# Kernel tuning notes

Measured on AMD Instinct MI355X. Metric: run time of the kernel, lower is better.

The kernel has to match this reference:

```python
import jax, jax.numpy as jnp
from jax import lax
import numpy as np

EPS = 1e-6
LN_EPS = 1e-3
B, T, F = 8, 2048, 80
STRIDE, NFILT = 2, 64
FEAT_P = 20              # ceil(80 / 4) after two stride-2 convs
CAPS_IN_N, CAPS_IN_D = 32, 8
CAPS_COV_N, CAPS_COV_D = 32, 8
CLASS_N, CAPS_CLS_D = 31, 8
WINDOW, LPAD, RPAD = 3, 1, 1
N_ITER = 3


def conv2d(x, w, b, stride):
    y = lax.conv_general_dilated(x, w, (stride, stride), 'SAME',
                                 dimension_numbers=('NHWC', 'HWIO', 'NHWC'))
    return y + b


def feat_mask(x, lengths, factor):
    # zero out time steps >= ceil(len/factor)
    S = x.shape[1]
    vl = jnp.ceil(lengths.astype(jnp.float32) / factor).astype(jnp.int32)
    m = (jnp.arange(S)[None, :] < vl[:, None]).astype(x.dtype)
    return x * m.reshape(m.shape + (1,) * (x.ndim - 2))


def squash(x, axis=-1):
    sq = jnp.sum(x * x, axis=axis, keepdims=True)
    return x * (sq / (1.0 + sq) / jnp.sqrt(sq + EPS))


def layernorm(x):
    mu = jnp.mean(x, -1, keepdims=True)
    var = jnp.var(x, -1, keepdims=True)
    return (x - mu) / jnp.sqrt(var + LN_EPS)


def window_concat(x):
    # [B,S,N,D] -> [B,S,N*WINDOW,D] (windowed context gather)
    S = x.shape[1]
    xp = jnp.pad(x, ((0, 0), (LPAD, RPAD), (0, 0), (0, 0)))
    return jnp.concatenate([xp[:, j:j + S] for j in range(WINDOW)], axis=2)


def dynamic_routing(u_hat, logit_mask):
    # u_hat: [B,S,I,O,D] -> v: [B,S,O,D]
    b0 = jnp.zeros(u_hat.shape[:4], u_hat.dtype)

    def body(b, _):
        c = jax.nn.softmax(b + logit_mask, axis=3)          # coupling coeffs
        s = jnp.einsum('bsio,bsiod->bsod', c, u_hat)
        v = squash(s, -1)
        b = b + jnp.einsum('bsiod,bsod->bsio', u_hat, v)    # agreement update
        return b, v

    _, vs = lax.scan(body, b0, None, length=N_ITER)
    return vs[-1]


def _forward(inputs, conv0_w1, conv0_b1, conv0_w2, conv0_b2,
             conv1_w1, conv1_b1, conv1_w2, conv1_b2,
             proj_w, proj_b, enc_w1, enc_b1, enc_w2, enc_b2,
             W0, B0, W1, B1, input_lengths):
    # --- CapsulationLayer: maxout conv feature extraction ---
    x = inputs[..., None]                                    # [B,T,F,1]
    x = jnp.maximum(conv2d(x, conv0_w1, conv0_b1, STRIDE),
                    conv2d(x, conv0_w2, conv0_b2, STRIDE))
    x = feat_mask(x, input_lengths, STRIDE)                  # [B,T/2,F/2,64]
    x = jnp.maximum(conv2d(x, conv1_w1, conv1_b1, STRIDE),
                    conv2d(x, conv1_w2, conv1_b2, STRIDE))
    x = feat_mask(x, input_lengths, STRIDE ** 2)             # [B,S,20,64]
    b, S = x.shape[0], x.shape[1]

    # --- primary capsules ---
    emb = x.reshape(b, S, FEAT_P * NFILT) @ proj_w + proj_b  # [B,S,32]
    emb = emb[..., None]                                     # [B,S,32,1]
    emb = jnp.maximum(conv2d(emb, enc_w1, enc_b1, 1),
                      conv2d(emb, enc_w2, enc_b2, 1))        # [B,S,32,8]
    emb = feat_mask(emb, input_lengths, STRIDE ** 2)
    emb = squash(emb, -1)
    emb = layernorm(emb.reshape(b, S, -1)).reshape(b, S, CAPS_IN_N, CAPS_IN_D)

    # --- caps layer 0: primary(windowed) -> convolution capsules ---
    win = window_concat(emb)                                 # [B,S,96,8]
    u = jnp.einsum('iodk,bsik->bsiod', W0, win) + B0[None, None]
    v = dynamic_routing(u, jnp.zeros((1, 1, 1, CAPS_COV_N), u.dtype))
    emb = layernorm(v.reshape(b, S, -1)).reshape(b, S, CAPS_COV_N, CAPS_COV_D)

    # --- caps layer 1: conv(windowed) -> class capsules (blank masked) ---
    win = window_concat(emb)                                 # [B,S,96,8]
    u = jnp.einsum('iodk,bsik->bsiod', W1, win) + B1[None, None]
    lm = jnp.concatenate([jnp.full((1, 1, 1, 1), -1e9, u.dtype),
                          jnp.zeros((1, 1, 1, CLASS_N - 1), u.dtype)], -1)
    v = dynamic_routing(u, lm)
    v = layernorm(v.reshape(b, S, -1)).reshape(b, S, CLASS_N, CAPS_CLS_D)

    # --- class capsule lengths + output layernorm ---
    out = jnp.sqrt(jnp.sum(v * v, -1) + EPS)                 # [B,S,31]
    return layernorm(out)


def setup_inputs() -> dict:
    key = jax.random.key(0)
    ks = list(jax.random.split(key, 24))
    n = lambda i, shape, s=0.1: jax.random.normal(ks[i], shape, jnp.float32) * s
    d = {
        'inputs': jax.random.normal(ks[0], (B, T, F), jnp.float32),
        'conv0_w1': n(1, (3, 3, 1, NFILT)), 'conv0_b1': n(2, (NFILT,)),
        'conv0_w2': n(3, (3, 3, 1, NFILT)), 'conv0_b2': n(4, (NFILT,)),
        'conv1_w1': n(5, (3, 3, NFILT, NFILT), 0.05), 'conv1_b1': n(6, (NFILT,)),
        'conv1_w2': n(7, (3, 3, NFILT, NFILT), 0.05), 'conv1_b2': n(8, (NFILT,)),
        'proj_w': n(9, (FEAT_P * NFILT, CAPS_IN_N), 0.02), 'proj_b': n(10, (CAPS_IN_N,)),
        'enc_w1': n(11, (3, 3, 1, CAPS_IN_D)), 'enc_b1': n(12, (CAPS_IN_D,)),
        'enc_w2': n(13, (3, 3, 1, CAPS_IN_D)), 'enc_b2': n(14, (CAPS_IN_D,)),
        'W0': n(15, (CAPS_IN_N * WINDOW, CAPS_COV_N, CAPS_COV_D, CAPS_IN_D)),
        'B0': n(16, (CAPS_IN_N * WINDOW, CAPS_COV_N, CAPS_COV_D)),
        'W1': n(17, (CAPS_COV_N * WINDOW, CLASS_N, CAPS_CLS_D, CAPS_COV_D)),
        'B1': n(18, (CAPS_COV_N * WINDOW, CLASS_N, CAPS_CLS_D)),
        'input_lengths': jax.random.randint(ks[19], (B,), T // 2, T + 1, jnp.int32),
    }
    return d


def reference(inputs, conv0_w1, conv0_b1, conv0_w2, conv0_b2,
              conv1_w1, conv1_b1, conv1_w2, conv1_b2,
              proj_w, proj_b, enc_w1, enc_b1, enc_w2, enc_b2,
              W0, B0, W1, B1, input_lengths):
    return _forward(inputs, conv0_w1, conv0_b1, conv0_w2, conv0_b2,
                    conv1_w1, conv1_b1, conv1_w2, conv1_b2,
                    proj_w, proj_b, enc_w1, enc_b1, enc_w2, enc_b2,
                    W0, B0, W1, B1, input_lengths)
```

## Files before the change

kernel.cpp:

```cpp
#include <hip/hip_runtime.h>

typedef unsigned short u16;
typedef unsigned int u32;
typedef short short8 __attribute__((ext_vector_type(8)));
typedef float f32x4 __attribute__((ext_vector_type(4)));
typedef _Float16 h2 __attribute__((ext_vector_type(2)));
typedef __fp16 fp16v2 __attribute__((ext_vector_type(2)));

#define DEV static __device__ __forceinline__

DEV float bf2f(u16 v) { return __uint_as_float((u32)v << 16); }
DEV u16 f2bf(float f) {
    u32 x = __float_as_uint(f);
    return (u16)((x + 0x7fffu + ((x >> 16) & 1u)) >> 16);
}
DEV u16 f2h(float f) {
    union { _Float16 h; u16 u; } c; c.h = (_Float16)f; return c.u;
}
DEV u32 pack2h(float a, float b) {
#if __has_builtin(__builtin_amdgcn_cvt_pkrtz)
    union { fp16v2 h; u32 u; } c;
    c.h = __builtin_amdgcn_cvt_pkrtz(a, b);
    return c.u;
#else
    union { u32 u; _Float16 h[2]; } c;
    c.h[0] = (_Float16)a; c.h[1] = (_Float16)b; return c.u;
#endif
}
DEV h2 u2h(u32 x) { union { u32 u; h2 h; } c; c.u = x; return c.h; }
DEV u32 h2u(h2 v) { union { h2 h; u32 u; } c; c.h = v; return c.u; }

#if __has_builtin(__builtin_amdgcn_fdot2)
DEV float dot2(u32 a, u32 b, float c) {
    return __builtin_amdgcn_fdot2(u2h(a), u2h(b), c, false);
}
#else
DEV float dot2(u32 a, u32 b, float c) {
    h2 ha = u2h(a), hb = u2h(b);
    c = fmaf((float)ha[0], (float)hb[0], c);
    return fmaf((float)ha[1], (float)hb[1], c);
}
#endif

constexpr int Bn = 8, Tn = 2048, Fn = 80, NF = 64;
constexpr int H1 = 1024, W1n = 40;
constexpr int Sn = 512,  W2n = 20;
constexpr int PK = 1280;
constexpr int I0 = 96;
constexpr int O0 = 32;
constexpr int O1 = 31;
constexpr int CPW = 52;
constexpr int NW0 = I0 * O0 * 8 * 8;
constexpr int NW1 = I0 * O1 * 8 * 8;
constexpr int KC1 = 576;

template <int CTRL>
DEV float dpp_mov(float x) {
    return __int_as_float(__builtin_amdgcn_update_dpp(
        0, __float_as_int(x), CTRL, 0xF, 0xF, true));
}
template <int CTRL>
DEV u32 dppu(u32 x) {
    return (u32)__builtin_amdgcn_update_dpp(0, (int)x, CTRL, 0xF, 0xF, true);
}
DEV float sum8(float x) {
    x += dpp_mov<0xB1>(x);
    x += dpp_mov<0x4E>(x);
    x += dpp_mov<0x141>(x);
    return x;
}
DEV u32 sum8h(u32 x) {
    x = h2u(u2h(x) + u2h(dppu<0xB1>(x)));
    x = h2u(u2h(x) + u2h(dppu<0x4E>(x)));
    x = h2u(u2h(x) + u2h(dppu<0x141>(x)));
    return x;
}

DEV float2 block_sum2(float a, float b, int tid, float* lds ) {
    #pragma unroll
    for (int m = 1; m < 64; m <<= 1) {
        a += __shfl_xor(a, m);
        b += __shfl_xor(b, m);
    }
    int wid = tid >> 6;
    __syncthreads();
    if ((tid & 63) == 0) { lds[wid * 2] = a; lds[wid * 2 + 1] = b; }
    __syncthreads();
    float ra = lds[0] + lds[2] + lds[4] + lds[6];
    float rb = lds[1] + lds[3] + lds[5] + lds[7];
    return make_float2(ra, rb);
}

__global__ void __launch_bounds__(256) k_prep(
        const float* __restrict__ w0, const float* __restrict__ w1c,
        const float* __restrict__ cw1, const float* __restrict__ cb1,
        const float* __restrict__ cw2, const float* __restrict__ cb2,
        u16* __restrict__ w0h, u16* __restrict__ w1h,
        u16* __restrict__ wt, float* __restrict__ biasi) {
    int idx = blockIdx.x * 256 + threadIdx.x;
    if (idx < NW0) w0h[idx] = f2h(w0[idx]);
    if (idx < NW1) w1h[idx] = f2h(w1c[idx]);
    if (idx < 128 * KC1) {
        int n = idx / KC1, k = idx - n * KC1;
        int c = n >> 1, s = n & 1;
        const float* w = s ? cw2 : cw1;
        wt[idx] = f2bf(w[k * 64 + c]);
    }
    if (idx < 128) {
        int c = idx >> 1, s = idx & 1;
        biasi[idx] = (s ? cb2 : cb1)[c];
    }
}

__global__ void __launch_bounds__(256) k_conv0(
        const float* __restrict__ in,
        const float* __restrict__ w1, const float* __restrict__ b1,
        const float* __restrict__ w2, const float* __restrict__ b2,
        const int* __restrict__ lens, u16* __restrict__ x1) {
    int idx = blockIdx.x * 256 + threadIdx.x;
    if (idx >= Bn * H1 * W1n * NF) return;
    int c = idx & 63;
    int rest = idx >> 6;
    int w = rest % W1n; rest /= W1n;
    int h = rest % H1;
    int b = rest / H1;
    float out = 0.f;
    int vl2 = (lens[b] + 1) >> 1;
    if (h < vl2) {
        float a1 = b1[c], a2 = b2[c];
        #pragma unroll
        for (int r = 0; r < 3; ++r) {
            int t = 2 * h + r;
            if (t < Tn) {
                #pragma unroll
                for (int q = 0; q < 3; ++q) {
                    int f = 2 * w + q;
                    if (f < Fn) {
                        float v = in[(b * Tn + t) * Fn + f];
                        int wi = (r * 3 + q) * 64 + c;
                        a1 = fmaf(v, w1[wi], a1);
                        a2 = fmaf(v, w2[wi], a2);
                    }
                }
            }
        }
        out = fmaxf(a1, a2);
    }
    x1[idx] = f2bf(out);
}

__global__ void __launch_bounds__(256) k_conv1(
        const u16* __restrict__ x1, const u16* __restrict__ wt,
        const float* __restrict__ biasi, const int* __restrict__ lens,
        u16* __restrict__ x2) {
    constexpr int LD = 40;
    __shared__ u16 Al[2][128 * LD];
    __shared__ u16 Bl[2][128 * LD];
    __shared__ float bs_lds[128];

    int tid = threadIdx.x;
    int m0 = blockIdx.x * 128;
    int b = m0 / 10240;
    int vl4 = (lens[b] + 3) >> 2;

    if (tid < 128) bs_lds[tid] = biasi[tid];

    int srow = tid >> 1;
    int shalf = tid & 1;
    int am = m0 + srow;
    int aw = am % 20;
    int ah = (am / 20) % 512;
    const u16* abase = x1 + (((size_t)b * 1024 + 2 * ah) * 40 + 2 * aw) * 64;
    const u16* bbase = wt + srow * KC1;

    const uint4 uz = make_uint4(0, 0, 0, 0);
    uint4 na0, na1, nb0, nb1;
    {
        const u16* ap = abase + shalf * 16;
        na0 = *(const uint4*)(ap);
        na1 = *(const uint4*)(ap + 8);
        const u16* bp = bbase + shalf * 16;
        nb0 = *(const uint4*)(bp);
        nb1 = *(const uint4*)(bp + 8);
    }
    {
        u16* awp = &Al[0][srow * LD + shalf * 16];
        *(uint4*)awp = na0; *(uint4*)(awp + 8) = na1;
        u16* bwp = &Bl[0][srow * LD + shalf * 16];
        *(uint4*)bwp = nb0; *(uint4*)(bwp + 8) = nb1;
    }
    __syncthreads();

    int lane = tid & 63;
    int wid = tid >> 6;
    int mw = wid & 1, nw = wid >> 1;
    int frow = lane & 15;
    int koff = (lane >> 4) * 8;

    f32x4 acc[4][4] = {};
    int buf = 0;

    #pragma unroll
    for (int kc = 0; kc < 18; ++kc) {
        if (kc < 17) {
            int kn = kc + 1;
            int rq = kn >> 1, ci0 = (kn & 1) * 32;
            int r = rq / 3, q = rq - 3 * r;
            bool v = (2 * ah + r < 1024) && (2 * aw + q < 40);
            const u16* ap = abase + (r * 40 + q) * 64 + ci0 + shalf * 16;
            na0 = v ? *(const uint4*)(ap) : uz;
            na1 = v ? *(const uint4*)(ap + 8) : uz;
            const u16* bp = bbase + kn * 32 + shalf * 16;
            nb0 = *(const uint4*)(bp);
            nb1 = *(const uint4*)(bp + 8);
        }
        const u16* Ar = &Al[buf][(mw * 64 + frow) * LD + koff];
        const u16* Br = &Bl[buf][(nw * 64 + frow) * LD + koff];
        short8 af[4], bfr[4];
        #pragma unroll
        for (int s = 0; s < 4; ++s) {
            af[s]  = *(const short8*)(Ar + s * 16 * LD);
            bfr[s] = *(const short8*)(Br + s * 16 * LD);
        }
        #pragma unroll
        for (int sm = 0; sm < 4; ++sm)
            #pragma unroll
            for (int sn = 0; sn < 4; ++sn)
                acc[sm][sn] = __builtin_amdgcn_mfma_f32_16x16x32_bf16(
                    af[sm], bfr[sn], acc[sm][sn], 0, 0, 0);
        if (kc < 17) {
            buf ^= 1;
            u16* awp = &Al[buf][srow * LD + shalf * 16];
            *(uint4*)awp = na0; *(uint4*)(awp + 8) = na1;
            u16* bwp = &Bl[buf][srow * LD + shalf * 16];
            *(uint4*)bwp = nb0; *(uint4*)(bwp + 8) = nb1;
            __syncthreads();
        }
    }

    int orow = (lane >> 4) * 4;
    int ncol = lane & 15;
    #pragma unroll
    for (int sm = 0; sm < 4; ++sm) {
        #pragma unroll
        for (int sn = 0; sn < 4; ++sn) {
            int np = nw * 64 + sn * 16 + ncol;
            float bia = bs_lds[np];
            #pragma unroll
            for (int r = 0; r < 4; ++r) {
                float v = acc[sm][sn][r] + bia;
                float o = fmaxf(v, dpp_mov<0xB1>(v));
                if (!(lane & 1)) {
                    int gm = m0 + mw * 64 + sm * 16 + orow + r;
                    int w = gm % 20;
                    int h = (gm / 20) % 512;
                    float res = (h >= vl4) ? 0.f : o;
                    x2[((size_t)(b * 512 + h) * 20 + w) * 64 + (np >> 1)] = f2bf(res);
                }
            }
        }
    }
}

__global__ void __launch_bounds__(256) k_proj(
        const u16* __restrict__ x2, const float* __restrict__ pw,
        const float* __restrict__ pb, float* __restrict__ proj) {
    int bs = blockIdx.x;
    int tid = threadIdx.x;
    int o = tid & 31, part = tid >> 5;
    const u16* row = &x2[(size_t)bs * PK];
    float acc = 0.f;
    int k0 = part * 160;
    #pragma unroll 8
    for (int k = 0; k < 160; ++k)
        acc = fmaf(bf2f(row[k0 + k]), pw[(k0 + k) * 32 + o], acc);
    __shared__ float red[256];
    red[tid] = acc;
    __syncthreads();
    if (tid < 32) {
        float s = 0.f;
        #pragma unroll
        for (int p = 0; p < 8; ++p) s += red[p * 32 + tid];
        proj[bs * 32 + tid] = s + pb[tid];
    }
}

__global__ void __launch_bounds__(256) k_enc(
        const float* __restrict__ proj,
        const float* __restrict__ ew1, const float* __restrict__ eb1,
        const float* __restrict__ ew2, const float* __restrict__ eb2,
        const int* __restrict__ lens, float* __restrict__ emb0) {
    int bs = blockIdx.x;
    int s = bs & (Sn - 1);
    int b = bs >> 9;
    int tid = threadIdx.x;
    __shared__ float rows[3][32];
    __shared__ float red[8];
    if (tid < 96) {
        int r = tid >> 5, n = tid & 31;
        int sr = s - 1 + r;
        rows[r][n] = (sr >= 0 && sr < Sn) ? proj[(b * Sn + sr) * 32 + n] : 0.f;
    }
    __syncthreads();

    int n = tid >> 3, d = tid & 7;
    float a1 = eb1[d], a2 = eb2[d];
    #pragma unroll
    for (int r = 0; r < 3; ++r) {
        #pragma unroll
        for (int q = 0; q < 3; ++q) {
            int nn = n - 1 + q;
            if (nn >= 0 && nn < 32) {
                float v = rows[r][nn];
                int wi = (r * 3 + q) * 8 + d;
                a1 = fmaf(v, ew1[wi], a1);
                a2 = fmaf(v, ew2[wi], a2);
            }
        }
    }
    float x = fmaxf(a1, a2);
    int vl4 = (lens[b] + 3) >> 2;
    if (s >= vl4) x = 0.f;

    float sq = sum8(x * x);
    x = x * (sq / (1.f + sq) * rsqrtf(sq + 1e-6f));

    float2 ss = block_sum2(x, x * x, tid, red);
    float mu = ss.x * (1.f / 256.f);
    float var = ss.y * (1.f / 256.f) - mu * mu;
    emb0[bs * 256 + tid] = (x - mu) * rsqrtf(var + 1e-3f);
}

__global__ void __launch_bounds__(256, 3) k_caps0(
        const float* __restrict__ embin, const u16* __restrict__ W0,
        const float* __restrict__ B0, float* __restrict__ embout) {
    int pb2 = blockIdx.x;
    int b = pb2 >> 8;
    int s0 = (pb2 & 255) << 1;
    int tid = threadIdx.x;
    int o = tid >> 3;

    __shared__ __align__(16) u32 win2[2][I0 * 4];
    __shared__ float blog[2][I0 * 33];
    __shared__ __align__(16) u32 cpk[2][O0 * CPW];
    __shared__ float red[8];
    u16* cph0 = (u16*)cpk[0];
    u16* cph1 = (u16*)cpk[1];

    for (int idx = tid; idx < 2 * I0 * 4; idx += 256) {
        int g = idx >= I0 * 4;
        int lidx = idx - g * I0 * 4;
        int i = lidx >> 2, kk = lidx & 3;
        int sr = s0 + g + (i >> 5) - 1;
        float a = 0.f, bv = 0.f;
        if (sr >= 0 && sr < Sn) {
            const float* p = &embin[(b * Sn + sr) * 256 + (i & 31) * 8 + kk * 2];
            a = p[0]; bv = p[1];
        }
        win2[g][lidx] = pack2h(a, bv);
    }
    for (int i = tid; i < 2 * I0 * 33; i += 256) blog[0][i] = 0.f;
    __syncthreads();

    u32 u_pk0[48], u_pk1[48];
    {
        const uint4* Wv = (const uint4*)W0;
        const uint4* wl0 = (const uint4*)win2[0];
        const uint4* wl1 = (const uint4*)win2[1];
        #pragma unroll
        for (int ii = 0; ii < 48; ++ii) {
            int i0 = 2 * ii, i1 = 2 * ii + 1;
            uint4 wv0 = Wv[i0 * 256 + tid];
            uint4 wv1 = Wv[i1 * 256 + tid];
            float bb0 = B0[i0 * 256 + tid];
            float bb1 = B0[i1 * 256 + tid];
            uint4 wa0 = wl0[i0], wa1 = wl0[i1];
            float a0 = bb0, a1 = bb1;
            a0 = dot2(wv0.x, wa0.x, a0);
            a0 = dot2(wv0.y, wa0.y, a0);
            a0 = dot2(wv0.z, wa0.z, a0);
            a0 = dot2(wv0.w, wa0.w, a0);
            a1 = dot2(wv1.x, wa1.x, a1);
            a1 = dot2(wv1.y, wa1.y, a1);
            a1 = dot2(wv1.z, wa1.z, a1);
            a1 = dot2(wv1.w, wa1.w, a1);
            u_pk0[ii] = pack2h(a0, a1);
            uint4 wb0 = wl1[i0], wb1 = wl1[i1];
            a0 = bb0; a1 = bb1;
            a0 = dot2(wv0.x, wb0.x, a0);
            a0 = dot2(wv0.y, wb0.y, a0);
            a0 = dot2(wv0.z, wb0.z, a0);
            a0 = dot2(wv0.w, wb0.w, a0);
            a1 = dot2(wv1.x, wb1.x, a1);
            a1 = dot2(wv1.y, wb1.y, a1);
            a1 = dot2(wv1.z, wb1.z, a1);
            a1 = dot2(wv1.w, wb1.w, a1);
            u_pk1[ii] = pack2h(a0, a1);
        }
    }

    float vv0 = 0.f, vv1 = 0.f;
    for (int it = 0; it < 3; ++it) {
        if (tid < 192) {
            int i = tid >> 1, hf = tid & 1;
            int o0 = hf * 16;
            #pragma unroll
            for (int g = 0; g < 2; ++g) {
                float ex[16];
                float ssum = 0.f;
                #pragma unroll
                for (int j = 0; j < 16; ++j) {
                    ex[j] = __expf(blog[g][i * 33 + o0 + j]);
                    ssum += ex[j];
                }
                ssum += dpp_mov<0xB1>(ssum);
                float inv = __builtin_amdgcn_rcpf(ssum);
                u16* cc = g ? cph1 : cph0;
                #pragma unroll
                for (int j = 0; j < 16; ++j)
                    cc[(o0 + j) * (CPW * 2) + i] = f2h(ex[j] * inv);
            }
        }
        __syncthreads();
        {
            float sv0 = 0.f, sv1 = 0.f;
            const uint4* cr0 = (const uint4*)&cpk[0][o * CPW];
            const uint4* cr1 = (const uint4*)&cpk[1][o * CPW];
            #pragma unroll
            for (int q4 = 0; q4 < 12; ++q4) {
                uint4 c0 = cr0[q4], c1 = cr1[q4];
                sv0 = dot2(u_pk0[q4 * 4 + 0], c0.x, sv0);
                sv0 = dot2(u_pk0[q4 * 4 + 1], c0.y, sv0);
                sv0 = dot2(u_pk0[q4 * 4 + 2], c0.z, sv0);
                sv0 = dot2(u_pk0[q4 * 4 + 3], c0.w, sv0);
                sv1 = dot2(u_pk1[q4 * 4 + 0], c1.x, sv1);
                sv1 = dot2(u_pk1[q4 * 4 + 1], c1.y, sv1);
                sv1 = dot2(u_pk1[q4 * 4 + 2], c1.z, sv1);
                sv1 = dot2(u_pk1[q4 * 4 + 3], c1.w, sv1);
            }
            float sq0 = sum8(sv0 * sv0);
            float sq1 = sum8(sv1 * sv1);
            vv0 = sv0 * (sq0 / (1.f + sq0) * rsqrtf(sq0 + 1e-6f));
            vv1 = sv1 * (sq1 / (1.f + sq1) * rsqrtf(sq1 + 1e-6f));
        }
        if (it < 2) {
            u32 va = pack2h(vv0, vv0), vb = pack2h(vv1, vv1);
            #pragma unroll
            for (int ii = 0; ii < 48; ++ii) {
                u32 p0 = sum8h(h2u(u2h(u_pk0[ii]) * u2h(va)));
                u32 p1 = sum8h(h2u(u2h(u_pk1[ii]) * u2h(vb)));
                if ((tid & 7) == 0) {
                    h2 q0 = u2h(p0), q1 = u2h(p1);
                    blog[0][(2 * ii) * 33 + o]     += (float)q0[0];
                    blog[0][(2 * ii + 1) * 33 + o] += (float)q0[1];
                    blog[1][(2 * ii) * 33 + o]     += (float)q1[0];
                    blog[1][(2 * ii + 1) * 33 + o] += (float)q1[1];
                }
            }
            __syncthreads();
        }
    }

    float2 ss = block_sum2(vv0, vv0 * vv0, tid, red);
    float mu = ss.x * (1.f / 256.f);
    float var = ss.y * (1.f / 256.f) - mu * mu;
    embout[(b * Sn + s0) * 256 + tid] = (vv0 - mu) * rsqrtf(var + 1e-3f);
    ss = block_sum2(vv1, vv1 * vv1, tid, red);
    mu = ss.x * (1.f / 256.f);
    var = ss.y * (1.f / 256.f) - mu * mu;
    embout[(b * Sn + s0 + 1) * 256 + tid] = (vv1 - mu) * rsqrtf(var + 1e-3f);
}

__global__ void __launch_bounds__(256, 3) k_caps1(
        const float* __restrict__ embin, const u16* __restrict__ W1,
        const float* __restrict__ B1, float* __restrict__ outp) {
    int pb2 = blockIdx.x;
    int b = pb2 >> 8;
    int s0 = (pb2 & 255) << 1;
    int tid = threadIdx.x;
    int o = tid >> 3, d = tid & 7;
    bool valid = (o < O1);
    int oc = valid ? o : (O1 - 1);
    int ocd = oc * 8 + d;

    __shared__ __align__(16) u32 win2[2][I0 * 4];
    __shared__ float blog[2][I0 * 33];
    __shared__ __align__(16) u32 cpk[2][O1 * CPW];
    __shared__ float red[8];
    __shared__ float lenb[2][O1];
    __shared__ float mv2[4];
    u16* cph0 = (u16*)cpk[0];
    u16* cph1 = (u16*)cpk[1];

    for (int idx = tid; idx < 2 * I0 * 4; idx += 256) {
        int g = idx >= I0 * 4;
        int lidx = idx - g * I0 * 4;
        int i = lidx >> 2, kk = lidx & 3;
        int sr = s0 + g + (i >> 5) - 1;
        float a = 0.f, bv = 0.f;
        if (sr >= 0 && sr < Sn) {
            const float* p = &embin[(b * Sn + sr) * 256 + (i & 31) * 8 + kk * 2];
            a = p[0]; bv = p[1];
        }
        win2[g][lidx] = pack2h(a, bv);
    }
    for (int i = tid; i < 2 * I0 * 33; i += 256) blog[0][i] = 0.f;
    for (int i = tid; i < CPW; i += 256) { cpk[0][i] = 0; cpk[1][i] = 0; }
    __syncthreads();

    u32 u_pk0[48], u_pk1[48];
    {
        const uint4* Wv = (const uint4*)W1;
        const uint4* wl0 = (const uint4*)win2[0];
        const uint4* wl1 = (const uint4*)win2[1];
        #pragma unroll
        for (int ii = 0; ii < 48; ++ii) {
            int i0 = 2 * ii, i1 = 2 * ii + 1;
            uint4 wv0 = Wv[i0 * 248 + ocd];
            uint4 wv1 = Wv[i1 * 248 + ocd];
            float bb0 = B1[i0 * 248 + ocd];
            float bb1 = B1[i1 * 248 + ocd];
            uint4 wa0 = wl0[i0], wa1 = wl0[i1];
            float a0 = bb0, a1 = bb1;
            a0 = dot2(wv0.x, wa0.x, a0);
            a0 = dot2(wv0.y, wa0.y, a0);
            a0 = dot2(wv0.z, wa0.z, a0);
            a0 = dot2(wv0.w, wa0.w, a0);
            a1 = dot2(wv1.x, wa1.x, a1);
            a1 = dot2(wv1.y, wa1.y, a1);
            a1 = dot2(wv1.z, wa1.z, a1);
            a1 = dot2(wv1.w, wa1.w, a1);
            u_pk0[ii] = pack2h(a0, a1);
            uint4 wb0 = wl1[i0], wb1 = wl1[i1];
            a0 = bb0; a1 = bb1;
            a0 = dot2(wv0.x, wb0.x, a0);
            a0 = dot2(wv0.y, wb0.y, a0);
            a0 = dot2(wv0.z, wb0.z, a0);
            a0 = dot2(wv0.w, wb0.w, a0);
            a1 = dot2(wv1.x, wb1.x, a1);
            a1 = dot2(wv1.y, wb1.y, a1);
            a1 = dot2(wv1.z, wb1.z, a1);
            a1 = dot2(wv1.w, wb1.w, a1);
            u_pk1[ii] = pack2h(a0, a1);
        }
    }

    float vv0 = 0.f, vv1 = 0.f;
    for (int it = 0; it < 3; ++it) {
        if (tid < 192) {
            int i = tid >> 1, hf = tid & 1;
            int lo = hf ? 16 : 1;
            #pragma unroll
            for (int g = 0; g < 2; ++g) {
                float ex[15];
                float ssum = 0.f;
                #pragma unroll
                for (int j = 0; j < 15; ++j) {
                    ex[j] = __expf(blog[g][i * 33 + lo + j]);
                    ssum += ex[j];
                }
                ssum += dpp_mov<0xB1>(ssum);
                float inv = __builtin_amdgcn_rcpf(ssum);
                u16* cc = g ? cph1 : cph0;
                #pragma unroll
                for (int j = 0; j < 15; ++j)
                    cc[(lo + j) * (CPW * 2) + i] = f2h(ex[j] * inv);
            }
        }
        __syncthreads();
        {
            float sv0 = 0.f, sv1 = 0.f;
            const uint4* cr0 = (const uint4*)&cpk[0][oc * CPW];
            const uint4* cr1 = (const uint4*)&cpk[1][oc * CPW];
            #pragma unroll
            for (int q4 = 0; q4 < 12; ++q4) {
                uint4 c0 = cr0[q4], c1 = cr1[q4];
                sv0 = dot2(u_pk0[q4 * 4 + 0], c0.x, sv0);
                sv0 = dot2(u_pk0[q4 * 4 + 1], c0.y, sv0);
                sv0 = dot2(u_pk0[q4 * 4 + 2], c0.z, sv0);
                sv0 = dot2(u_pk0[q4 * 4 + 3], c0.w, sv0);
                sv1 = dot2(u_pk1[q4 * 4 + 0], c1.x, sv1);
                sv1 = dot2(u_pk1[q4 * 4 + 1], c1.y, sv1);
                sv1 = dot2(u_pk1[q4 * 4 + 2], c1.z, sv1);
                sv1 = dot2(u_pk1[q4 * 4 + 3], c1.w, sv1);
            }
            float sq0 = sum8(sv0 * sv0);
            float sq1 = sum8(sv1 * sv1);
            vv0 = sv0 * (sq0 / (1.f + sq0) * rsqrtf(sq0 + 1e-6f));
            vv1 = sv1 * (sq1 / (1.f + sq1) * rsqrtf(sq1 + 1e-6f));
            if (!valid) { vv0 = 0.f; vv1 = 0.f; }
        }
        if (it < 2) {
            u32 va = pack2h(vv0, vv0), vb = pack2h(vv1, vv1);
            #pragma unroll
            for (int ii = 0; ii < 48; ++ii) {
                u32 p0 = sum8h(h2u(u2h(u_pk0[ii]) * u2h(va)));
                u32 p1 = sum8h(h2u(u2h(u_pk1[ii]) * u2h(vb)));
                if ((tid & 7) == 0 && valid) {
                    h2 q0 = u2h(p0), q1 = u2h(p1);
                    blog[0][(2 * ii) * 33 + o]     += (float)q0[0];
                    blog[0][(2 * ii + 1) * 33 + o] += (float)q0[1];
                    blog[1][(2 * ii) * 33 + o]     += (float)q1[0];
                    blog[1][(2 * ii + 1) * 33 + o] += (float)q1[1];
                }
            }
            __syncthreads();
        }
    }

    float2 ss = block_sum2(vv0, vv0 * vv0, tid, red);
    float mu = ss.x * (1.f / 248.f);
    float var = ss.y * (1.f / 248.f) - mu * mu;
    float y0 = (vv0 - mu) * rsqrtf(var + 1e-3f);
    ss = block_sum2(vv1, vv1 * vv1, tid, red);
    mu = ss.x * (1.f / 248.f);
    var = ss.y * (1.f / 248.f) - mu * mu;
    float y1 = (vv1 - mu) * rsqrtf(var + 1e-3f);

    float sq0 = sum8(y0 * y0);
    float sq1 = sum8(y1 * y1);
    if (valid && (tid & 7) == 0) {
        lenb[0][o] = sqrtf(sq0 + 1e-6f);
        lenb[1][o] = sqrtf(sq1 + 1e-6f);
    }
    __syncthreads();

    if (tid < 2) {
        float s1 = 0.f, s2 = 0.f;
        for (int oo = 0; oo < O1; ++oo) { float t = lenb[tid][oo]; s1 += t; s2 += t * t; }
        float m2 = s1 / 31.f;
        mv2[tid * 2] = m2;
        mv2[tid * 2 + 1] = rsqrtf(s2 / 31.f - m2 * m2 + 1e-3f);
    }
    __syncthreads();
    if (tid < O1) {
        outp[(size_t)(b * Sn + s0) * O1 + tid] = (lenb[0][tid] - mv2[0]) * mv2[1];
        outp[(size_t)(b * Sn + s0 + 1) * O1 + tid] = (lenb[1][tid] - mv2[2]) * mv2[3];
    }
}

extern "C" void kernel_launch(void* const* d_in, const int* in_sizes, int n_in,
                              void* d_out, int out_size, void* d_ws, size_t ws_size,
                              hipStream_t stream) {
    const float* inputs = (const float*)d_in[0];
    const float* c0w1 = (const float*)d_in[1];
    const float* c0b1 = (const float*)d_in[2];
    const float* c0w2 = (const float*)d_in[3];
    const float* c0b2 = (const float*)d_in[4];
    const float* c1w1 = (const float*)d_in[5];
    const float* c1b1 = (const float*)d_in[6];
    const float* c1w2 = (const float*)d_in[7];
    const float* c1b2 = (const float*)d_in[8];
    const float* pw   = (const float*)d_in[9];
    const float* pb   = (const float*)d_in[10];
    const float* ew1  = (const float*)d_in[11];
    const float* eb1  = (const float*)d_in[12];
    const float* ew2  = (const float*)d_in[13];
    const float* eb2  = (const float*)d_in[14];
    const float* W0   = (const float*)d_in[15];
    const float* B0   = (const float*)d_in[16];
    const float* W1   = (const float*)d_in[17];
    const float* B1   = (const float*)d_in[18];
    const int* lens = (const int*)d_in[19];

    char* ws = (char*)d_ws;
    u16*   x1    = (u16*)(ws);
    u16*   x2    = (u16*)(ws + 41943040);
    float* proj  = (float*)(ws + 52428800);
    float* emb0  = (float*)(ws + 52953088);
    float* emb1  = (float*)(ws + 57147392);
    u16*   W0h   = (u16*)(ws + 61341696);
    u16*   W1h   = (u16*)(ws + 61734912);
    u16*   wt    = (u16*)(ws + 62115840);
    float* biasi = (float*)(ws + 62263296);

    k_prep<<<(NW0 + 255) / 256, 256, 0, stream>>>(
        W0, W1, c1w1, c1b1, c1w2, c1b2, W0h, W1h, wt, biasi);
    k_conv0<<<(Bn * H1 * W1n * NF) / 256, 256, 0, stream>>>(
        inputs, c0w1, c0b1, c0w2, c0b2, lens, x1);
    k_conv1<<<640, 256, 0, stream>>>(x1, wt, biasi, lens, x2);
    k_proj<<<Bn * Sn, 256, 0, stream>>>(x2, pw, pb, proj);
    k_enc<<<Bn * Sn, 256, 0, stream>>>(proj, ew1, eb1, ew2, eb2, lens, emb0);
    k_caps0<<<Bn * Sn / 2, 256, 0, stream>>>(emb0, W0h, B0, emb1);
    k_caps1<<<Bn * Sn / 2, 256, 0, stream>>>(emb1, W1h, B1, (float*)d_out);
}
```

Measured before the change: 437.0 us.

## Restructure conv0 to one block per output row with LDS-staged input

The first maxout conv now runs one block per (batch, output row). Each block stages the three input rows it needs in shared memory and keeps the nine per-channel weights of both filters in registers. Each thread then computes ten output columns for its channel. This removes the redundant global loads of inputs and weights and the per-element index division of the old one-thread-per-output layout. In exchange the grid is far smaller and each thread does more serial work.

Result: faster. 353.7 us, median of 2 (-19.1%).

```diff
diff --git a/kernel.cpp b/kernel.cpp
--- a/kernel.cpp
+++ b/kernel.cpp
@@ -117,36 +117,50 @@
         const float* __restrict__ w1, const float* __restrict__ b1,
         const float* __restrict__ w2, const float* __restrict__ b2,
         const int* __restrict__ lens, u16* __restrict__ x1) {
-    int idx = blockIdx.x * 256 + threadIdx.x;
-    if (idx >= Bn * H1 * W1n * NF) return;
-    int c = idx & 63;
-    int rest = idx >> 6;
-    int w = rest % W1n; rest /= W1n;
-    int h = rest % H1;
-    int b = rest / H1;
-    float out = 0.f;
+    __shared__ float srow[3][82];
+    int blk = blockIdx.x;
+    int h = blk & (H1 - 1);
+    int b = blk >> 10;
+    int tid = threadIdx.x;
+
+    for (int idx = tid; idx < 3 * 82; idx += 256) {
+        int r = idx / 82, f = idx - r * 82;
+        int t = 2 * h + r;
+        float v = 0.f;
+        if (t < Tn && f < Fn) v = in[(b * Tn + t) * Fn + f];
+        srow[r][f] = v;
+    }
+    __syncthreads();
+
+    int c = tid & 63;
+    int wq = tid >> 6;
+    float wr1[9], wr2[9];
+    #pragma unroll
+    for (int j = 0; j < 9; ++j) {
+        wr1[j] = w1[j * 64 + c];
+        wr2[j] = w2[j * 64 + c];
+    }
+    float bb1 = b1[c], bb2 = b2[c];
     int vl2 = (lens[b] + 1) >> 1;
-    if (h < vl2) {
-        float a1 = b1[c], a2 = b2[c];
+    bool masked = (h >= vl2);
+
+    u16* outbase = x1 + ((size_t)(b * H1 + h) * W1n) * 64 + c;
+    #pragma unroll
+    for (int p = 0; p < 10; ++p) {
+        int w = wq * 10 + p;
+        float a1 = bb1, a2 = bb2;
         #pragma unroll
         for (int r = 0; r < 3; ++r) {
-            int t = 2 * h + r;
-            if (t < Tn) {
-                #pragma unroll
-                for (int q = 0; q < 3; ++q) {
-                    int f = 2 * w + q;
-                    if (f < Fn) {
-                        float v = in[(b * Tn + t) * Fn + f];
-                        int wi = (r * 3 + q) * 64 + c;
-                        a1 = fmaf(v, w1[wi], a1);
-                        a2 = fmaf(v, w2[wi], a2);
-                    }
-                }
-            }
-        }
-        out = fmaxf(a1, a2);
-    }
-    x1[idx] = f2bf(out);
+            #pragma unroll
+            for (int q = 0; q < 3; ++q) {
+                float v = srow[r][2 * w + q];
+                a1 = fmaf(v, wr1[r * 3 + q], a1);
+                a2 = fmaf(v, wr2[r * 3 + q], a2);
+            }
+        }
+        float out = masked ? 0.f : fmaxf(a1, a2);
+        outbase[w * 64] = f2bf(out);
+    }
 }
 
 __global__ void __launch_bounds__(256) k_conv1(
@@ -676,7 +690,7 @@
 
     k_prep<<<(NW0 + 255) / 256, 256, 0, stream>>>(
         W0, W1, c1w1, c1b1, c1w2, c1b2, W0h, W1h, wt, biasi);
-    k_conv0<<<(Bn * H1 * W1n * NF) / 256, 256, 0, stream>>>(
+    k_conv0<<<Bn * H1, 256, 0, stream>>>(
         inputs, c0w1, c0b1, c0w2, c0b2, lens, x1);
     k_conv1<<<640, 256, 0, stream>>>(x1, wt, biasi, lens, x2);
     k_proj<<<Bn * Sn, 256, 0, stream>>>(x2, pw, pb, proj);
```
